# Performance work log

Measured on AMD Instinct MI355X. Metric: run time of the kernel, lower is better.

The kernel has to match this reference:

```python
import jax, jax.numpy as jnp
import numpy as np

D = 1024
H = 16
HD = D // H
S = 2048
B = 2
HID = D * 7 // 2  # 3584


def _linear_params(key, din, dout):
    kw, kb = jax.random.split(key)
    bound = 1.0 / np.sqrt(din)
    W = jax.random.uniform(kw, (dout, din), jnp.float32, -bound, bound)
    b = jax.random.uniform(kb, (dout,), jnp.float32, -bound, bound)
    return W, b


def setup_inputs() -> dict:
    key = jax.random.key(0)
    ks = jax.random.split(key, 9)
    x = jax.random.normal(ks[0], (B, S, D), jnp.float32)
    pos_emb = 0.02 * jax.random.normal(ks[1], (1, S, D), jnp.float32)
    q_w, q_b = _linear_params(ks[2], D, D)
    k_w, k_b = _linear_params(ks[3], D, D)
    v_w, v_b = _linear_params(ks[4], D, D)
    o_w, o_b = _linear_params(ks[5], D, D)
    in_w, in_b = _linear_params(ks[6], D, HID)
    gate_w, gate_b = _linear_params(ks[7], D, HID)
    out_w, out_b = _linear_params(ks[8], HID, D)
    norm1_w = jnp.ones((D,), jnp.float32)
    norm2_w = jnp.ones((D,), jnp.float32)
    return dict(x=x, pos_emb=pos_emb, norm1_w=norm1_w, norm2_w=norm2_w,
                q_w=q_w, q_b=q_b, k_w=k_w, k_b=k_b, v_w=v_w, v_b=v_b,
                o_w=o_w, o_b=o_b, in_w=in_w, in_b=in_b,
                gate_w=gate_w, gate_b=gate_b, out_w=out_w, out_b=out_b)


def _rmsnorm(x, w, eps=1e-6):
    return x * jax.lax.rsqrt(jnp.mean(x * x, axis=-1, keepdims=True) + eps) * w


def _attn(x, q_w, q_b, k_w, k_b, v_w, v_b, o_w, o_b):
    b, s, _ = x.shape
    q = (x @ q_w.T + q_b).reshape(b, s, H, HD)
    k = (x @ k_w.T + k_b).reshape(b, s, H, HD)
    v = (x @ v_w.T + v_b).reshape(b, s, H, HD)
    scores = jnp.einsum('bqhd,bkhd->bhqk', q, k) / jnp.sqrt(jnp.float32(HD))
    causal = jnp.tril(jnp.ones((s, s), bool))  # True = keep
    scores = jnp.where(causal, scores, -jnp.inf)
    p = jax.nn.softmax(scores, axis=-1)
    o = jnp.einsum('bhqk,bkhd->bqhd', p, v).reshape(b, s, D)
    return o @ o_w.T + o_b


def _mlp(x, in_w, in_b, gate_w, gate_b, out_w, out_b):
    gate = jax.nn.silu(x @ gate_w.T + gate_b)
    h = gate * (x @ in_w.T + in_b)
    return h @ out_w.T + out_b


def reference(x, pos_emb, norm1_w, norm2_w, q_w, q_b, k_w, k_b, v_w, v_b,
              o_w, o_b, in_w, in_b, gate_w, gate_b, out_w, out_b):
    x = x + pos_emb
    x = x + _attn(_rmsnorm(x, norm1_w), q_w, q_b, k_w, k_b, v_w, v_b, o_w, o_b)
    x = x + _mlp(_rmsnorm(x, norm2_w), in_w, in_b, gate_w, gate_b, out_w, out_b)
    return x
```

## Files before the change

kernel.cpp:

```cpp
#include <hip/hip_runtime.h>

typedef __attribute__((ext_vector_type(4))) float f32x4;
typedef __attribute__((ext_vector_type(8))) short bf16x8;
typedef unsigned short u16;

constexpr int kB = 2, kS = 2048, kD = 1024, kH = 16, kHD = 64, kHID = 3584;
constexpr int kN = kB * kS;

__device__ __forceinline__ u16 f2bf(float f) {
  unsigned u = __float_as_uint(f);
  u = (u + 0x7FFFu + ((u >> 16) & 1u)) >> 16;
  return (u16)u;
}
__device__ __forceinline__ float bf2f(u16 v) {
  return __uint_as_float((unsigned)v << 16);
}

__device__ __forceinline__ float rowmax16(float v) {
  int t;
  t = __builtin_amdgcn_update_dpp(0, __float_as_int(v), 0x121, 0xf, 0xf, true);
  v = fmaxf(v, __int_as_float(t));
  t = __builtin_amdgcn_update_dpp(0, __float_as_int(v), 0x122, 0xf, 0xf, true);
  v = fmaxf(v, __int_as_float(t));
  t = __builtin_amdgcn_update_dpp(0, __float_as_int(v), 0x124, 0xf, 0xf, true);
  v = fmaxf(v, __int_as_float(t));
  t = __builtin_amdgcn_update_dpp(0, __float_as_int(v), 0x128, 0xf, 0xf, true);
  v = fmaxf(v, __int_as_float(t));
  return v;
}

#define AS1(p) ((const __attribute__((address_space(1))) void*)(p))
#define AS3(p) ((__attribute__((address_space(3))) void*)(p))

__global__ __launch_bounds__(256) void k_prep(
    const float* __restrict__ x, const float* __restrict__ pos,
    const float* __restrict__ w, float* __restrict__ xr, u16* __restrict__ xn) {
  const int n = blockIdx.x, t = threadIdx.x, s = n & (kS - 1);
  float4 a = ((const float4*)(x + (size_t)n * kD))[t];
  float4 p = ((const float4*)(pos + (size_t)s * kD))[t];
  a.x += p.x; a.y += p.y; a.z += p.z; a.w += p.w;
  ((float4*)(xr + (size_t)n * kD))[t] = a;
  float ss = a.x*a.x + a.y*a.y + a.z*a.z + a.w*a.w;
#pragma unroll
  for (int off = 1; off < 64; off <<= 1) ss += __shfl_xor(ss, off);
  __shared__ float red[4];
  if ((t & 63) == 0) red[t >> 6] = ss;
  __syncthreads();
  float rs = rsqrtf((red[0] + red[1] + red[2] + red[3]) * (1.0f / kD) + 1e-6f);
  float4 wv = ((const float4*)w)[t];
  ushort4 o;
  o.x = f2bf(a.x * rs * wv.x); o.y = f2bf(a.y * rs * wv.y);
  o.z = f2bf(a.z * rs * wv.z); o.w = f2bf(a.w * rs * wv.w);
  ((ushort4*)(xn + (size_t)n * kD))[t] = o;
}

__global__ __launch_bounds__(256) void k_rms2(
    const float* __restrict__ xin, const float* __restrict__ w, u16* __restrict__ xn) {
  const int n = blockIdx.x, t = threadIdx.x;
  float4 a = ((const float4*)(xin + (size_t)n * kD))[t];
  float ss = a.x*a.x + a.y*a.y + a.z*a.z + a.w*a.w;
#pragma unroll
  for (int off = 1; off < 64; off <<= 1) ss += __shfl_xor(ss, off);
  __shared__ float red[4];
  if ((t & 63) == 0) red[t >> 6] = ss;
  __syncthreads();
  float rs = rsqrtf((red[0] + red[1] + red[2] + red[3]) * (1.0f / kD) + 1e-6f);
  float4 wv = ((const float4*)w)[t];
  ushort4 o;
  o.x = f2bf(a.x * rs * wv.x); o.y = f2bf(a.y * rs * wv.y);
  o.z = f2bf(a.z * rs * wv.z); o.w = f2bf(a.w * rs * wv.w);
  ((ushort4*)(xn + (size_t)n * kD))[t] = o;
}

__device__ __forceinline__ void cvt4(const float* __restrict__ s, u16* __restrict__ d, int j) {
  float4 v = ((const float4*)s)[j];
  ushort4 o;
  o.x = f2bf(v.x); o.y = f2bf(v.y); o.z = f2bf(v.z); o.w = f2bf(v.w);
  ((ushort4*)d)[j] = o;
}

__global__ __launch_bounds__(256) void k_wprep(
    const float* __restrict__ q_w, const float* __restrict__ k_w,
    const float* __restrict__ v_w, const float* __restrict__ o_w,
    const float* __restrict__ in_w, const float* __restrict__ gate_w,
    const float* __restrict__ out_w,
    const float* __restrict__ q_b, const float* __restrict__ k_b,
    const float* __restrict__ v_b,
    u16* __restrict__ W, float* __restrict__ bqkv) {
  const int i = blockIdx.x * 256 + threadIdx.x;
  if (i < 262144)       cvt4(q_w,    W + 0,        i);
  else if (i < 524288)  cvt4(k_w,    W + 1048576,  i - 262144);
  else if (i < 786432)  cvt4(v_w,    W + 2097152,  i - 524288);
  else if (i < 1048576) cvt4(o_w,    W + 3145728,  i - 786432);
  else if (i < 1966080) cvt4(in_w,   W + 4194304,  i - 1048576);
  else if (i < 2883584) cvt4(gate_w, W + 7864320,  i - 1966080);
  else if (i < 3801088) cvt4(out_w,  W + 11534336, i - 2883584);
  else {
    const int j = i - 3801088;
    const float* src = j < 256 ? q_b : (j < 512 ? k_b : v_b);
    ((float4*)bqkv)[j] = ((const float4*)src)[j & 255];
  }
}

template <int MODE, int BM>
__global__ __launch_bounds__(256) void k_gemm(
    const u16* __restrict__ A, const u16* __restrict__ Bw,
    const float* __restrict__ bias, const void* extra,
    void* outp, int M, int N, int K, int nbx) {
  constexpr int ASEG = BM / 16;
  constexpr int NSEG = ASEG + 8;
  constexpr int WROWS = BM / 2;
  constexpr int MF = BM / 32;
  __shared__ __align__(16) u16 As[2][BM * 32];
  __shared__ __align__(16) u16 Bs[2][128 * 32];
  const int tid = threadIdx.x, lane = tid & 63, wv_ = tid >> 6;
  const int lr = lane & 15, lg = lane >> 4;
  const int chunk = gridDim.x >> 3;
  const int sid = (blockIdx.x & 7) * chunk + (blockIdx.x >> 3);
  const int brow = (sid / nbx) * BM, bcol = (sid % nbx) * 128;
  const int wr = wv_ >> 1, wc = wv_ & 1;

  const f32x4 zz = {0.f, 0.f, 0.f, 0.f};
  f32x4 acc[MF][4];
#pragma unroll
  for (int m = 0; m < MF; m++)
#pragma unroll
    for (int n = 0; n < 4; n++) acc[m][n] = zz;

  auto stage = [&](int kt, int buf) {
#pragma unroll
    for (int i = 0; i < NSEG / 4; ++i) {
      const int seg = i * 4 + wv_;
      const int rsub = (seg < ASEG) ? seg : seg - ASEG;
      const int row = rsub * 16 + (lane >> 2), cs = lane & 3;
      if (seg < ASEG) {
        __builtin_amdgcn_global_load_lds(AS1(A + (size_t)(brow + row) * K + kt + cs * 8),
                                         AS3((char*)&As[buf][0] + (size_t)seg * 1024), 16, 0, 0);
      } else {
        __builtin_amdgcn_global_load_lds(AS1(Bw + (size_t)(bcol + row) * K + kt + cs * 8),
                                         AS3((char*)&Bs[buf][0] + (size_t)(seg - ASEG) * 1024), 16, 0, 0);
      }
    }
  };

  stage(0, 0);
  __syncthreads();
  for (int kt = 0; kt < K; kt += 32) {
    const int cur = (kt >> 5) & 1;
    if (kt + 32 < K) stage(kt + 32, cur ^ 1);
    bf16x8 af[MF], bfr[4];
#pragma unroll
    for (int m = 0; m < MF; m++) af[m] = *(const bf16x8*)&As[cur][(wr * WROWS + m * 16 + lr) * 32 + lg * 8];
#pragma unroll
    for (int n = 0; n < 4; n++) bfr[n] = *(const bf16x8*)&Bs[cur][(wc * 64 + n * 16 + lr) * 32 + lg * 8];
#pragma unroll
    for (int m = 0; m < MF; m++)
#pragma unroll
      for (int n = 0; n < 4; n++)
        acc[m][n] = __builtin_amdgcn_mfma_f32_16x16x32_bf16(af[m], bfr[n], acc[m][n], 0, 0, 0);
    __syncthreads();
  }

#pragma unroll
  for (int m = 0; m < MF; m++) {
    const int row0 = brow + wr * WROWS + m * 16 + lg * 4;
#pragma unroll
    for (int n = 0; n < 4; n++) {
      const int col = bcol + wc * 64 + n * 16 + lr;
      const float bv = bias[col];
#pragma unroll
      for (int r = 0; r < 4; r++) {
        const size_t idx = (size_t)(row0 + r) * N + col;
        float v = acc[m][n][r] + bv;
        if (MODE == 0) {
          ((u16*)outp)[idx] = f2bf(v);
        } else if (MODE == 1) {
          ((float*)outp)[idx] = v + ((const float*)extra)[idx];
        } else {
          float g = v / (1.0f + __expf(-v));
          ((u16*)outp)[idx] = f2bf(g * bf2f(((const u16*)extra)[idx]));
        }
      }
    }
  }
}

__global__ __launch_bounds__(512) void k_attn(
    const u16* __restrict__ qkv, u16* __restrict__ attn_o) {
  __shared__ __align__(16) u16 Ks[2][64 * 64];
  __shared__ __align__(16) u16 Vt[64 * 64];
  __shared__ __align__(16) u16 Pl[8][16 * 64];

  const int tid = threadIdx.x, lane = tid & 63, w = tid >> 6;
  const int g = w >> 2, wi = w & 3;
  const int lr = lane & 15, lg = lane >> 4;
  const int p = blockIdx.x, bh = blockIdx.y;
  const int b = bh >> 4, h = bh & 15;
  const int qb = g == 0 ? 31 - p : p;
  const size_t base = (size_t)b * kS;
  const f32x4 zz = {0.f, 0.f, 0.f, 0.f};
  bf16x8 vones;
#pragma unroll
  for (int j = 0; j < 8; j++) vones[j] = (short)0x3F80;

  bf16x8 qf[2];
#pragma unroll
  for (int ks = 0; ks < 2; ks++)
    qf[ks] = *(const bf16x8*)&qkv[(base + qb * 64 + wi * 16 + lr) * 3072 + h * 64 + ks * 32 + lg * 8];

  f32x4 oacc[4], lacc = zz;
  float mrow[4];
#pragma unroll
  for (int nb = 0; nb < 4; nb++) oacc[nb] = zz;
#pragma unroll
  for (int r = 0; r < 4; r++) mrow[r] = -1e30f;

  const int kvloc = (w << 3) + (lane >> 3);
  const int kchv = ((lane & 7) ^ (lane >> 3)) * 8;
  auto issueK = [&](int t, int buf) {
    __builtin_amdgcn_global_load_lds(
        AS1(qkv + (base + t * 64 + kvloc) * 3072 + 1024 + h * 64 + kchv),
        AS3((char*)&Ks[buf][0] + w * 1024 + (size_t)lane * 16), 16, 0, 0);
  };
  const int srow = tid >> 3, dc = (tid & 7) * 8;
  int4 vr;
  auto issueV = [&](int t) {
    vr = *(const int4*)&qkv[(base + t * 64 + srow) * 3072 + 2048 + h * 64 + dc];
  };
  auto commitV = [&]() {
    const u16* ve = (const u16*)&vr;
#pragma unroll
    for (int j = 0; j < 8; j++) {
      const int d = dc + j;
      *(u16*)((char*)Vt + ((d * 128 + srow * 2) ^ ((d & 7) << 4))) = ve[j];
    }
  };

  auto compute = [&](int t, int buf) {
    const char* kbuf = (const char*)&Ks[buf][0];
    const bool masked = (t == qb);
    f32x4 sc[4];
#pragma unroll
    for (int hn = 0; hn < 4; hn++) sc[hn] = zz;
#pragma unroll
    for (int hn = 0; hn < 4; hn++) {
      const int krow = hn * 16 + lr;
#pragma unroll
      for (int ks = 0; ks < 2; ks++) {
        const int bo = (krow * 128 + (ks * 32 + lg * 8) * 2) ^ ((krow & 7) << 4);
        bf16x8 kf = *(const bf16x8*)(kbuf + bo);
        sc[hn] = __builtin_amdgcn_mfma_f32_16x16x32_bf16(qf[ks], kf, sc[hn], 0, 0, 0);
      }
    }
    float alpha[4];
#pragma unroll
    for (int r = 0; r < 4; r++) {
      const int qa = qb * 64 + wi * 16 + lg * 4 + r;
      float s0 = sc[0][r] * 0.125f, s1 = sc[1][r] * 0.125f;
      float s2 = sc[2][r] * 0.125f, s3 = sc[3][r] * 0.125f;
      if (masked) {
        if (t * 64 + lr > qa) s0 = -1e30f;
        if (t * 64 + 16 + lr > qa) s1 = -1e30f;
        if (t * 64 + 32 + lr > qa) s2 = -1e30f;
        if (t * 64 + 48 + lr > qa) s3 = -1e30f;
      }
      float mx = rowmax16(fmaxf(fmaxf(s0, s1), fmaxf(s2, s3)));
      const float mnew = fmaxf(mrow[r], mx);
      alpha[r] = __expf(mrow[r] - mnew);
      mrow[r] = mnew;
      sc[0][r] = __expf(s0 - mnew); sc[1][r] = __expf(s1 - mnew);
      sc[2][r] = __expf(s2 - mnew); sc[3][r] = __expf(s3 - mnew);
    }
#pragma unroll
    for (int nb = 0; nb < 4; nb++)
#pragma unroll
      for (int r = 0; r < 4; r++) oacc[nb][r] *= alpha[r];
#pragma unroll
    for (int r = 0; r < 4; r++) lacc[r] *= alpha[r];
    char* pw = (char*)&Pl[w][0];
#pragma unroll
    for (int hn = 0; hn < 4; hn++)
#pragma unroll
      for (int r = 0; r < 4; r++) {
        const int prow = lg * 4 + r, pcol = hn * 16 + lr;
        *(u16*)(pw + ((prow * 128 + pcol * 2) ^ ((prow & 7) << 4))) = f2bf(sc[hn][r]);
      }
    bf16x8 pf[2];
#pragma unroll
    for (int ks = 0; ks < 2; ks++)
      pf[ks] = *(const bf16x8*)((const char*)pw + ((lr * 128 + (ks * 32 + lg * 8) * 2) ^ ((lr & 7) << 4)));
#pragma unroll
    for (int nb = 0; nb < 4; nb++) {
      const int vrow = nb * 16 + lr;
#pragma unroll
      for (int ks = 0; ks < 2; ks++) {
        const int bo = (vrow * 128 + (ks * 32 + lg * 8) * 2) ^ ((vrow & 7) << 4);
        bf16x8 vf = *(const bf16x8*)((const char*)Vt + bo);
        oacc[nb] = __builtin_amdgcn_mfma_f32_16x16x32_bf16(pf[ks], vf, oacc[nb], 0, 0, 0);
      }
    }
#pragma unroll
    for (int ks = 0; ks < 2; ks++)
      lacc = __builtin_amdgcn_mfma_f32_16x16x32_bf16(pf[ks], vones, lacc, 0, 0, 0);
  };

  const int nt = 32 - p;
  issueV(0);
  issueK(0, 0);
  commitV();
  __syncthreads();
  for (int t = 0; t < nt; ++t) {
    const bool hn = (t + 1 < nt);
    if (hn) { issueV(t + 1); issueK(t + 1, (t + 1) & 1); }
    if (g == 0 || t <= p) compute(t, t & 1);
    __syncthreads();
    if (hn) commitV();
    __syncthreads();
  }

#pragma unroll
  for (int nb = 0; nb < 4; nb++)
#pragma unroll
    for (int r = 0; r < 4; r++) {
      const int q = qb * 64 + wi * 16 + lg * 4 + r;
      attn_o[(base + q) * kD + h * 64 + nb * 16 + lr] = f2bf(oacc[nb][r] / lacc[r]);
    }
}

constexpr size_t OFF_XR   = 0;
constexpr size_t OFF_XN1  = OFF_XR  + (size_t)kN * kD * 4;
constexpr size_t OFF_XN2  = OFF_XN1 + (size_t)kN * kD * 2;
constexpr size_t OFF_W    = OFF_XN2 + (size_t)kN * kD * 2;
constexpr size_t OFF_BQKV = OFF_W + 15204352ull * 2;
constexpr size_t OFF_ACT  = OFF_BQKV + 3072 * 4;

extern "C" void kernel_launch(void* const* d_in, const int* in_sizes, int n_in,
                              void* d_out, int out_size, void* d_ws, size_t ws_size,
                              hipStream_t stream) {
  const float* x     = (const float*)d_in[0];
  const float* pos   = (const float*)d_in[1];
  const float* n1w   = (const float*)d_in[2];
  const float* n2w   = (const float*)d_in[3];
  const float* q_w   = (const float*)d_in[4];
  const float* q_b   = (const float*)d_in[5];
  const float* k_w   = (const float*)d_in[6];
  const float* k_b   = (const float*)d_in[7];
  const float* v_w   = (const float*)d_in[8];
  const float* v_b   = (const float*)d_in[9];
  const float* o_w   = (const float*)d_in[10];
  const float* o_b   = (const float*)d_in[11];
  const float* in_w  = (const float*)d_in[12];
  const float* in_b  = (const float*)d_in[13];
  const float* gate_w= (const float*)d_in[14];
  const float* gate_b= (const float*)d_in[15];
  const float* out_w = (const float*)d_in[16];
  const float* out_b = (const float*)d_in[17];
  float* outf = (float*)d_out;
  char* ws = (char*)d_ws;

  float* xr   = (float*)(ws + OFF_XR);
  u16*   xn1  = (u16*)(ws + OFF_XN1);
  u16*   xn2  = (u16*)(ws + OFF_XN2);
  u16*   W    = (u16*)(ws + OFF_W);
  float* bqkv = (float*)(ws + OFF_BQKV);
  u16*   qkv  = (u16*)(ws + OFF_ACT);
  u16*   attn_o = (u16*)(ws + OFF_ACT + (size_t)kN * 3072 * 2);
  u16*   inoutb = (u16*)(ws + OFF_ACT);
  u16*   hb     = (u16*)(ws + OFF_ACT + (size_t)kN * kHID * 2);

  u16* Wq   = W + 0;
  u16* Wo   = W + 3145728;
  u16* Win  = W + 4194304;
  u16* Wg   = W + 7864320;
  u16* Wout = W + 11534336;

  k_prep<<<kN, 256, 0, stream>>>(x, pos, n1w, xr, xn1);
  k_wprep<<<14851, 256, 0, stream>>>(q_w, k_w, v_w, o_w, in_w, gate_w, out_w,
                                     q_b, k_b, v_b, W, bqkv);

  k_gemm<0, 128><<<768, 256, 0, stream>>>(xn1, Wq, bqkv, nullptr, qkv, kN, 3072, kD, 24);

  k_attn<<<dim3(16, kB * kH), 512, 0, stream>>>(qkv, attn_o);

  k_gemm<1, 64><<<512, 256, 0, stream>>>(attn_o, Wo, o_b, xr, outf, kN, kD, kD, 8);

  k_rms2<<<kN, 256, 0, stream>>>(outf, n2w, xn2);

  k_gemm<0, 128><<<896, 256, 0, stream>>>(xn2, Win, in_b, nullptr, inoutb, kN, kHID, kD, 28);
  k_gemm<3, 128><<<896, 256, 0, stream>>>(xn2, Wg, gate_b, inoutb, hb, kN, kHID, kD, 28);

  k_gemm<1, 64><<<512, 256, 0, stream>>>(hb, Wout, out_b, outf, outf, kN, kD, kHID, 8);
}
```

Before: 489.4 us.

## Fuse MLP in and gate GEMMs into one kernel, relax GEMM barriers

```diff
diff --git a/kernel.cpp b/kernel.cpp
--- a/kernel.cpp
+++ b/kernel.cpp
@@ -14,6 +14,20 @@
 }
 __device__ __forceinline__ float bf2f(u16 v) {
   return __uint_as_float((unsigned)v << 16);
+}
+
+template <int N>
+__device__ __forceinline__ void waitcnt_vm() {
+  if constexpr (N == 0) asm volatile("s_waitcnt vmcnt(0)" ::: "memory");
+  else if constexpr (N == 3) asm volatile("s_waitcnt vmcnt(3)" ::: "memory");
+  else if constexpr (N == 4) asm volatile("s_waitcnt vmcnt(4)" ::: "memory");
+  else if constexpr (N == 5) asm volatile("s_waitcnt vmcnt(5)" ::: "memory");
+  else if constexpr (N == 6) asm volatile("s_waitcnt vmcnt(6)" ::: "memory");
+}
+__device__ __forceinline__ void barrier_raw() {
+  __builtin_amdgcn_sched_barrier(0);
+  __builtin_amdgcn_s_barrier();
+  __builtin_amdgcn_sched_barrier(0);
 }
 
 __device__ __forceinline__ float rowmax16(float v) {
@@ -109,6 +123,7 @@
     void* outp, int M, int N, int K, int nbx) {
   constexpr int ASEG = BM / 16;
   constexpr int NSEG = ASEG + 8;
+  constexpr int GPW = NSEG / 4;
   constexpr int WROWS = BM / 2;
   constexpr int MF = BM / 32;
   __shared__ __align__(16) u16 As[2][BM * 32];
@@ -129,7 +144,7 @@
 
   auto stage = [&](int kt, int buf) {
 #pragma unroll
-    for (int i = 0; i < NSEG / 4; ++i) {
+    for (int i = 0; i < GPW; ++i) {
       const int seg = i * 4 + wv_;
       const int rsub = (seg < ASEG) ? seg : seg - ASEG;
       const int row = rsub * 16 + (lane >> 2), cs = lane & 3;
@@ -144,10 +159,12 @@
   };
 
   stage(0, 0);
-  __syncthreads();
   for (int kt = 0; kt < K; kt += 32) {
     const int cur = (kt >> 5) & 1;
-    if (kt + 32 < K) stage(kt + 32, cur ^ 1);
+    const bool nx = (kt + 32 < K);
+    if (nx) { stage(kt + 32, cur ^ 1); waitcnt_vm<GPW>(); }
+    else    { waitcnt_vm<0>(); }
+    barrier_raw();
     bf16x8 af[MF], bfr[4];
 #pragma unroll
     for (int m = 0; m < MF; m++) af[m] = *(const bf16x8*)&As[cur][(wr * WROWS + m * 16 + lr) * 32 + lg * 8];
@@ -158,7 +175,7 @@
 #pragma unroll
       for (int n = 0; n < 4; n++)
         acc[m][n] = __builtin_amdgcn_mfma_f32_16x16x32_bf16(af[m], bfr[n], acc[m][n], 0, 0, 0);
-    __syncthreads();
+    barrier_raw();
   }
 
 #pragma unroll
@@ -174,12 +191,86 @@
         float v = acc[m][n][r] + bv;
         if (MODE == 0) {
           ((u16*)outp)[idx] = f2bf(v);
-        } else if (MODE == 1) {
+        } else {
           ((float*)outp)[idx] = v + ((const float*)extra)[idx];
-        } else {
-          float g = v / (1.0f + __expf(-v));
-          ((u16*)outp)[idx] = f2bf(g * bf2f(((const u16*)extra)[idx]));
         }
+      }
+    }
+  }
+}
+
+__global__ __launch_bounds__(256, 2) void k_mlp(
+    const u16* __restrict__ A, const u16* __restrict__ Bi, const u16* __restrict__ Bg,
+    const float* __restrict__ bias_i, const float* __restrict__ bias_g,
+    u16* __restrict__ outp, int M, int N, int K, int nbx) {
+  __shared__ __align__(16) u16 AsT[2][128 * 32];
+  __shared__ __align__(16) u16 BiT[2][128 * 32];
+  __shared__ __align__(16) u16 BgT[2][128 * 32];
+  const int tid = threadIdx.x, lane = tid & 63, wv_ = tid >> 6;
+  const int lr = lane & 15, lg = lane >> 4;
+  const int chunk = gridDim.x >> 3;
+  const int sid = (blockIdx.x & 7) * chunk + (blockIdx.x >> 3);
+  const int brow = (sid / nbx) * 128, bcol = (sid % nbx) * 128;
+  const int wr = wv_ >> 1, wc = wv_ & 1;
+
+  const f32x4 zz = {0.f, 0.f, 0.f, 0.f};
+  f32x4 accI[4][4], accG[4][4];
+#pragma unroll
+  for (int m = 0; m < 4; m++)
+#pragma unroll
+    for (int n = 0; n < 4; n++) { accI[m][n] = zz; accG[m][n] = zz; }
+
+  auto stage = [&](int kt, int buf) {
+#pragma unroll
+    for (int i = 0; i < 6; ++i) {
+      const int seg = i * 4 + wv_;
+      const int rsub = seg & 7;
+      const int row = rsub * 16 + (lane >> 2), cs = lane & 3;
+      const size_t goff = (size_t)(seg < 8 ? brow + row : bcol + row) * K + kt + cs * 8;
+      const u16* src = (seg < 8) ? A : (seg < 16 ? Bi : Bg);
+      char* dst = (seg < 8) ? (char*)&AsT[buf][0] : (seg < 16 ? (char*)&BiT[buf][0] : (char*)&BgT[buf][0]);
+      __builtin_amdgcn_global_load_lds(AS1(src + goff), AS3(dst + (size_t)rsub * 1024), 16, 0, 0);
+    }
+  };
+
+  stage(0, 0);
+  for (int kt = 0; kt < K; kt += 32) {
+    const int cur = (kt >> 5) & 1;
+    const bool nx = (kt + 32 < K);
+    if (nx) { stage(kt + 32, cur ^ 1); waitcnt_vm<6>(); }
+    else    { waitcnt_vm<0>(); }
+    barrier_raw();
+    bf16x8 af[4], bfi[4], bfg[4];
+#pragma unroll
+    for (int m = 0; m < 4; m++) af[m] = *(const bf16x8*)&AsT[cur][(wr * 64 + m * 16 + lr) * 32 + lg * 8];
+#pragma unroll
+    for (int n = 0; n < 4; n++) {
+      bfi[n] = *(const bf16x8*)&BiT[cur][(wc * 64 + n * 16 + lr) * 32 + lg * 8];
+      bfg[n] = *(const bf16x8*)&BgT[cur][(wc * 64 + n * 16 + lr) * 32 + lg * 8];
+    }
+#pragma unroll
+    for (int m = 0; m < 4; m++)
+#pragma unroll
+      for (int n = 0; n < 4; n++) {
+        accI[m][n] = __builtin_amdgcn_mfma_f32_16x16x32_bf16(af[m], bfi[n], accI[m][n], 0, 0, 0);
+        accG[m][n] = __builtin_amdgcn_mfma_f32_16x16x32_bf16(af[m], bfg[n], accG[m][n], 0, 0, 0);
+      }
+    barrier_raw();
+  }
+
+#pragma unroll
+  for (int m = 0; m < 4; m++) {
+    const int row0 = brow + wr * 64 + m * 16 + lg * 4;
+#pragma unroll
+    for (int n = 0; n < 4; n++) {
+      const int col = bcol + wc * 64 + n * 16 + lr;
+      const float bi = bias_i[col], bg = bias_g[col];
+#pragma unroll
+      for (int r = 0; r < 4; r++) {
+        const float vi = accI[m][n][r] + bi;
+        const float vg = accG[m][n][r] + bg;
+        const float g = vg / (1.0f + __expf(-vg));
+        outp[(size_t)(row0 + r) * N + col] = f2bf(g * vi);
       }
     }
   }
@@ -365,8 +456,7 @@
   float* bqkv = (float*)(ws + OFF_BQKV);
   u16*   qkv  = (u16*)(ws + OFF_ACT);
   u16*   attn_o = (u16*)(ws + OFF_ACT + (size_t)kN * 3072 * 2);
-  u16*   inoutb = (u16*)(ws + OFF_ACT);
-  u16*   hb     = (u16*)(ws + OFF_ACT + (size_t)kN * kHID * 2);
+  u16*   hb     = (u16*)(ws + OFF_ACT);
 
   u16* Wq   = W + 0;
   u16* Wo   = W + 3145728;
@@ -386,8 +476,7 @@
 
   k_rms2<<<kN, 256, 0, stream>>>(outf, n2w, xn2);
 
-  k_gemm<0, 128><<<896, 256, 0, stream>>>(xn2, Win, in_b, nullptr, inoutb, kN, kHID, kD, 28);
-  k_gemm<3, 128><<<896, 256, 0, stream>>>(xn2, Wg, gate_b, inoutb, hb, kN, kHID, kD, 28);
+  k_mlp<<<896, 256, 0, stream>>>(xn2, Win, Wg, in_b, gate_b, hb, kN, kHID, kD, 28);
 
   k_gemm<1, 64><<<512, 256, 0, stream>>>(hb, Wout, out_b, outf, outf, kN, kD, kHID, 8);
 }
```

After: 606.5 us. 1.24x slower.
